# Kernel tuning notes

Measured on AMD Instinct MI355X. Metric: run time of the kernel, lower is better.

Reference implementation:

```python
import jax, jax.numpy as jnp
import numpy as np

H, F = 4, 32          # num_of_heads, num_out_features
HF = H * F            # 128
F_IN = 128
EDGE_DIM = 64
HIDDEN = 256
B = 64
MLE = 1500
N = B * MLE           # 96000
E = 600000
LN_EPS = 1e-5


def setup_inputs() -> dict:
    key = jax.random.key(0)
    ks = jax.random.split(key, 20)

    def glorot(k, shape):
        fan_in, fan_out = shape[-2], shape[-1]
        lim = np.sqrt(6.0 / (fan_in + fan_out))
        return jax.random.uniform(k, shape, jnp.float32, -lim, lim)

    inp = {
        "in_nodes_features": jax.random.normal(ks[0], (N, F_IN), jnp.float32),
        "edge_index": jax.random.randint(ks[1], (2, E), 0, N),
        "edges": jax.random.normal(ks[2], (E, EDGE_DIM), jnp.float32),
        "instructions": jax.random.normal(ks[3], (B, HIDDEN), jnp.float32),
        "batch_ids": jax.random.randint(ks[4], (E,), 0, B),
        "max_local_entity": MLE,
        # parameters (stored as [in, out]; torch Linear is x @ W.T)
        "W_proj": glorot(ks[5], (F_IN, HF)),
        "W_edge": glorot(ks[6], (EDGE_DIM, HF)),
        "W_src_ins": glorot(ks[7], (HIDDEN, HF)),
        "b_src_ins": jnp.zeros((HF,), jnp.float32),
        "W_trg_ins": glorot(ks[8], (HIDDEN, HF)),
        "b_trg_ins": jnp.zeros((HF,), jnp.float32),
        "W_edge_ins": glorot(ks[9], (HIDDEN, HF)),
        "b_edge_ins": jnp.zeros((HF,), jnp.float32),
        "a_src": glorot(ks[10], (1, H, F)),
        "a_trg": glorot(ks[11], (1, H, F)),
        "a_edge": glorot(ks[12], (1, H, F)),
        "bias": jnp.zeros((HF,), jnp.float32),
        "W_skip": glorot(ks[13], (F_IN, HF)),
        "ln_gamma": jnp.ones((2 * HF,), jnp.float32),
        "ln_beta": jnp.zeros((2 * HF,), jnp.float32),
    }
    return inp


def _segment_softmax(scores, seg_idx, num_nodes):
    # scores: [E, H]; softmax over edges sharing the same seg_idx node
    s = scores - jax.lax.stop_gradient(scores.max())  # global-max shift, as in original
    e = jnp.exp(s)
    denom = jax.ops.segment_sum(e, seg_idx, num_segments=num_nodes)  # [N, H]
    return (e / (denom[seg_idx] + 1e-16))[..., None]  # [E, H, 1]


def _branch(proj, lift_idx, agg_idx, scores_per_edge, x, W_skip, bias, num_nodes):
    att = _segment_softmax(scores_per_edge, agg_idx, num_nodes)          # [E,H,1]
    weighted = proj[lift_idx] * att                                      # [E,H,F]
    out = jax.ops.segment_sum(weighted, agg_idx, num_segments=num_nodes) # [N,H,F]
    out = out + (x @ W_skip).reshape(num_nodes, H, F)                    # skip (F != F_in path)
    out = out.reshape(num_nodes, HF) + bias                              # concat heads + bias
    return out


def reference(in_nodes_features, edge_index, edges, instructions, batch_ids,
              max_local_entity, W_proj, W_edge, W_src_ins, b_src_ins,
              W_trg_ins, b_trg_ins, W_edge_ins, b_edge_ins,
              a_src, a_trg, a_edge, bias, W_skip, ln_gamma, ln_beta):
    x = in_nodes_features                      # dropout disabled (eval / p=0)
    num_nodes = x.shape[0]
    b = instructions.shape[0]
    src_idx, trg_idx = edge_index[0], edge_index[1]

    proj = (x @ W_proj).reshape(num_nodes, H, F)           # [N,H,F]
    eproj = (edges @ W_edge).reshape(-1, H, F)             # [E,H,F]

    def bridge(Wi, bi):  # instruction -> per-node [N,H,F]
        br = instructions @ Wi + bi                        # [B,HF]
        br = jnp.broadcast_to(br[:, None, :], (b, max_local_entity, HF))
        return br.reshape(num_nodes, H, F)

    src_br = bridge(W_src_ins, b_src_ins)
    trg_br = bridge(W_trg_ins, b_trg_ins)
    edge_br = (instructions @ W_edge_ins + b_edge_ins)[batch_ids].reshape(-1, H, F)

    scores_source = (proj * a_src * src_br).sum(-1)        # [N,H]
    scores_target = (proj * a_trg * trg_br).sum(-1)        # [N,H]
    scores_edge = (eproj * a_edge * edge_br).sum(-1)       # [E,H]

    scores_per_edge = jax.nn.leaky_relu(
        scores_source[src_idx] + scores_target[trg_idx] + scores_edge,
        negative_slope=0.2)                                # [E,H]

    # direction == 'all': aggregate src->trg and trg->src
    trg_feats = _branch(proj, src_idx, trg_idx, scores_per_edge, x, W_skip, bias, num_nodes)
    src_feats = _branch(proj, trg_idx, src_idx, scores_per_edge, x, W_skip, bias, num_nodes)

    out = jnp.concatenate([src_feats, trg_feats], axis=1)  # [N, 2*HF]
    mu = out.mean(-1, keepdims=True)
    var = ((out - mu) ** 2).mean(-1, keepdims=True)
    return (out - mu) * jax.lax.rsqrt(var + LN_EPS) * ln_gamma + ln_beta
```

## Files before the change

### kernel.cpp

```cpp
#include <hip/hip_runtime.h>
#include <stdint.h>

typedef unsigned short ushortT;
typedef __attribute__((ext_vector_type(8))) short short8;
typedef __attribute__((ext_vector_type(4))) float float4_;

#define HH 4
#define FF 32
#define HFD 128
#define F_IN 128
#define EDGE_DIM 64
#define HIDDEN 256
#define BB 64
#define MLE 1500
#define NN 96000
#define EEc 600000
#define CAP 32

__device__ __forceinline__ float bf_lo(uint32_t u){ return __uint_as_float(u << 16); }
__device__ __forceinline__ float bf_hi(uint32_t u){ return __uint_as_float(u & 0xffff0000u); }
__device__ __forceinline__ uint32_t f2bf(float f){
    uint32_t u = __float_as_uint(f);
    return (u + 0x7fffu + ((u >> 16) & 1u)) >> 16;
}
__device__ __forceinline__ short8 cvt8(const float* p){
    float4_ x0 = *(const float4_*)p;
    float4_ x1 = *(const float4_*)(p + 4);
    short8 r;
    r[0]=(short)f2bf(x0[0]); r[1]=(short)f2bf(x0[1]); r[2]=(short)f2bf(x0[2]); r[3]=(short)f2bf(x0[3]);
    r[4]=(short)f2bf(x1[0]); r[5]=(short)f2bf(x1[1]); r[6]=(short)f2bf(x1[2]); r[7]=(short)f2bf(x1[3]);
    return r;
}

__global__ void k_bridge(const float* ins, const float* Wsrc, const float* bsrc,
                         const float* Wtrg, const float* btrg,
                         const float* Wedg, const float* bedg,
                         const float* a_src, const float* a_trg, const float* a_edge,
                         const float* W_edge,
                         float* csrc, float* ctrg, float* Mout)
{
    __shared__ float ins_s[HIDDEN];
    __shared__ float ce_s[HFD];
    int b = blockIdx.x, t = threadIdx.x;
    const float* ip = ins + b * HIDDEN;
    ins_s[t]       = ip[t];
    ins_s[t + 128] = ip[t + 128];
    __syncthreads();
    float as = 0.f, at = 0.f, ae = 0.f;
    for (int k = 0; k < HIDDEN; k++){
        float iv = ins_s[k];
        as += iv * Wsrc[k*HFD + t];
        at += iv * Wtrg[k*HFD + t];
        ae += iv * Wedg[k*HFD + t];
    }
    csrc[b*HFD + t] = (as + bsrc[t]) * a_src[t];
    ctrg[b*HFD + t] = (at + btrg[t]) * a_trg[t];
    ce_s[t] = (ae + bedg[t]) * a_edge[t];
    __syncthreads();
    #pragma unroll
    for (int rep = 0; rep < 2; rep++){
        int idx = t + rep * 128;
        int d = idx >> 2, h = idx & 3;
        float acc = 0.f;
        #pragma unroll
        for (int f = 0; f < FF; f++)
            acc += W_edge[d*HFD + h*FF + f] * ce_s[h*FF + f];
        Mout[b*256 + h*64 + d] = acc;
    }
}

__global__ void k_transpose(const float* Wp, const float* Wsk, ushortT* WcatT)
{
    int idx = blockIdx.x * 256 + threadIdx.x;
    int c = idx >> 7;
    int d = idx & 127;
    float v = (c < 128) ? Wp[d*128 + c] : Wsk[d*128 + (c - 128)];
    WcatT[c*128 + d] = (ushortT)f2bf(v);
}

__global__ __launch_bounds__(256) void k_gemm(const float* x, const ushortT* WcatT,
                                              const float* csrc, const float* ctrg,
                                              ushortT* proj, ushortT* skip,
                                              float* s_src, float* s_trg)
{
    int t = threadIdx.x;
    int w = t >> 6, lane = t & 63;
    int q = lane >> 4, n16 = lane & 15;
    size_t node = (size_t)blockIdx.x * 64 + w * 16 + n16;

    float4_ acc[16];
    #pragma unroll
    for (int j = 0; j < 16; j++) acc[j] = (float4_){0.f, 0.f, 0.f, 0.f};

    #pragma unroll
    for (int kk = 0; kk < 4; kk++){
        short8 bfrag = cvt8(x + node * 128 + kk*32 + q*8);
        #pragma unroll
        for (int j = 0; j < 16; j++){
            short8 afrag = *(const short8*)(WcatT + (size_t)(j*16 + n16) * 128 + kk*32 + q*8);
            acc[j] = __builtin_amdgcn_mfma_f32_16x16x32_bf16(afrag, bfrag, acc[j], 0, 0, 0);
        }
    }

    #pragma unroll
    for (int j = 0; j < 16; j++){
        uint32_t p0 = f2bf(acc[j][0]) | (f2bf(acc[j][1]) << 16);
        uint32_t p1 = f2bf(acc[j][2]) | (f2bf(acc[j][3]) << 16);
        ushortT* base = (j < 8) ? (proj + node*128 + j*16 + q*4)
                                : (skip + node*128 + (j-8)*16 + q*4);
        uint2 pv; pv.x = p0; pv.y = p1;
        *(uint2*)base = pv;
    }

    int b = (int)(node / MLE);
    const float* cs = csrc + b * HFD;
    const float* ct = ctrg + b * HFD;
    float ps[4] = {0,0,0,0}, pt[4] = {0,0,0,0};
    #pragma unroll
    for (int j = 0; j < 8; j++){
        int h = j >> 1;
        #pragma unroll
        for (int r = 0; r < 4; r++){
            int c = j*16 + q*4 + r;
            ps[h] += acc[j][r] * cs[c];
            pt[h] += acc[j][r] * ct[c];
        }
    }
    #pragma unroll
    for (int m = 16; m < 64; m <<= 1){
        #pragma unroll
        for (int hh = 0; hh < 4; hh++){
            ps[hh] += __shfl_xor(ps[hh], m, 64);
            pt[hh] += __shfl_xor(pt[hh], m, 64);
        }
    }
    float vs = (q == 0) ? ps[0] : (q == 1) ? ps[1] : (q == 2) ? ps[2] : ps[3];
    float vt = (q == 0) ? pt[0] : (q == 1) ? pt[1] : (q == 2) ? pt[2] : pt[3];
    s_src[node*4 + q] = vs;
    s_trg[node*4 + q] = vt;
}

__global__ __launch_bounds__(256) void k_edges(const int* eidx, const int* bids,
    const float* edges, const float* M, const float* s_src, const float* s_trg,
    float* ex, int* cnt_src, int* cnt_trg, uint32_t* adj_src, uint32_t* adj_trg)
{
    int t = threadIdx.x;
    int wave = t >> 6, l = t & 63;
    int g = l >> 4, s = l & 15;
    int eb = (blockIdx.x * 4 + wave) * 16;

    float4_ ev[4];
    int bidv[4];
    #pragma unroll
    for (int i = 0; i < 4; i++){
        int r = i*4 + g;
        ev[i]   = *(const float4_*)(edges + (size_t)(eb + r) * 64 + s*4);
        bidv[i] = bids[eb + r];
    }

    float p00=0.f,p01=0.f,p02=0.f,p03=0.f;
    float p10=0.f,p11=0.f,p12=0.f,p13=0.f;
    float p20=0.f,p21=0.f,p22=0.f,p23=0.f;
    float p30=0.f,p31=0.f,p32=0.f,p33=0.f;
    #pragma unroll
    for (int i = 0; i < 4; i++){
        const float* Mb = M + (size_t)bidv[i] * 256;
        float4_ m0 = *(const float4_*)(Mb +   0 + s*4);
        float4_ m1 = *(const float4_*)(Mb +  64 + s*4);
        float4_ m2 = *(const float4_*)(Mb + 128 + s*4);
        float4_ m3 = *(const float4_*)(Mb + 192 + s*4);
        float4_ e4 = ev[i];
        float d0 = e4[0]*m0[0] + e4[1]*m0[1] + e4[2]*m0[2] + e4[3]*m0[3];
        float d1 = e4[0]*m1[0] + e4[1]*m1[1] + e4[2]*m1[2] + e4[3]*m1[3];
        float d2 = e4[0]*m2[0] + e4[1]*m2[1] + e4[2]*m2[2] + e4[3]*m2[3];
        float d3 = e4[0]*m3[0] + e4[1]*m3[1] + e4[2]*m3[2] + e4[3]*m3[3];
        if (i == 0){ p00=d0; p01=d1; p02=d2; p03=d3; }
        if (i == 1){ p10=d0; p11=d1; p12=d2; p13=d3; }
        if (i == 2){ p20=d0; p21=d1; p22=d2; p23=d3; }
        if (i == 3){ p30=d0; p31=d1; p32=d2; p33=d3; }
    }

    #pragma unroll
    for (int mm = 1; mm < 16; mm <<= 1){
        p00 += __shfl_xor(p00, mm, 64); p01 += __shfl_xor(p01, mm, 64);
        p02 += __shfl_xor(p02, mm, 64); p03 += __shfl_xor(p03, mm, 64);
        p10 += __shfl_xor(p10, mm, 64); p11 += __shfl_xor(p11, mm, 64);
        p12 += __shfl_xor(p12, mm, 64); p13 += __shfl_xor(p13, mm, 64);
        p20 += __shfl_xor(p20, mm, 64); p21 += __shfl_xor(p21, mm, 64);
        p22 += __shfl_xor(p22, mm, 64); p23 += __shfl_xor(p23, mm, 64);
        p30 += __shfl_xor(p30, mm, 64); p31 += __shfl_xor(p31, mm, 64);
        p32 += __shfl_xor(p32, mm, 64); p33 += __shfl_xor(p33, mm, 64);
    }

    int i_sel = s >> 2;
    int h_sel = s & 3;
    float q0 = h_sel==0 ? p00 : h_sel==1 ? p01 : h_sel==2 ? p02 : p03;
    float q1 = h_sel==0 ? p10 : h_sel==1 ? p11 : h_sel==2 ? p12 : p13;
    float q2 = h_sel==0 ? p20 : h_sel==1 ? p21 : h_sel==2 ? p22 : p23;
    float q3 = h_sel==0 ? p30 : h_sel==1 ? p31 : h_sel==2 ? p32 : p33;
    float se = i_sel==0 ? q0 : i_sel==1 ? q1 : i_sel==2 ? q2 : q3;

    int e   = eb + i_sel*4 + g;
    int src = eidx[e];
    int trg = eidx[EEc + e];
    float sc = s_src[(size_t)src*4 + h_sel] + s_trg[(size_t)trg*4 + h_sel] + se;
    sc = sc > 0.f ? sc : 0.2f * sc;
    ex[(size_t)e*4 + h_sel] = __expf(sc);

    if (h_sel == 0){
        int sl = atomicAdd(&cnt_src[src], 1);
        if (sl < CAP) adj_src[(size_t)src*CAP + sl] = (uint32_t)e;
        int sl2 = atomicAdd(&cnt_trg[trg], 1);
        if (sl2 < CAP) adj_trg[(size_t)trg*CAP + sl2] = (uint32_t)e;
    }
}

__global__ __launch_bounds__(256) void k_agg(const ushortT* proj, const ushortT* skip,
    const float* bias, const float* ex, const int* eidx,
    const int* cnt_src, const int* cnt_trg,
    const uint32_t* adj_src, const uint32_t* adj_trg,
    const float* gamma, const float* beta, float* out)
{
    __shared__ int   sh_nbr[2][4][CAP];
    __shared__ float sh_ev [2][4][CAP*4];

    int wave = threadIdx.x >> 6, lane = threadIdx.x & 63;
    int n = blockIdx.x * 4 + wave;
    int h = lane >> 4;

    int cnt0 = cnt_src[n]; if (cnt0 > CAP) cnt0 = CAP;
    int cnt1 = cnt_trg[n]; if (cnt1 > CAP) cnt1 = CAP;

    if (lane < cnt0){
        int e = (int)adj_src[(size_t)n * CAP + lane];
        sh_nbr[0][wave][lane] = eidx[EEc + e];
        *(float4_*)&sh_ev[0][wave][lane*4] = *(const float4_*)(ex + (size_t)e*4);
    }
    if (lane < cnt1){
        int e = (int)adj_trg[(size_t)n * CAP + lane];
        sh_nbr[1][wave][lane] = eidx[e];
        *(float4_*)&sh_ev[1][wave][lane*4] = *(const float4_*)(ex + (size_t)e*4);
    }

    uint32_t sv = ((const uint32_t*)(skip + (size_t)n * 128))[lane];
    float b0 = bias[2*lane], b1 = bias[2*lane + 1];

    __syncthreads();

    float sk0 = bf_lo(sv) + b0;
    float sk1 = bf_hi(sv) + b1;

    float a0 = 0.f, a1 = 0.f, ad = 0.f;
    #pragma unroll 4
    for (int i = 0; i < cnt0; i++){
        int nbr  = sh_nbr[0][wave][i];
        float ev = sh_ev[0][wave][i*4 + h];
        uint32_t pv = ((const uint32_t*)(proj + (size_t)nbr * 128))[lane];
        a0 += ev * bf_lo(pv);
        a1 += ev * bf_hi(pv);
        ad += ev;
    }
    float inv = 1.f / (ad + 1e-16f);
    float f0 = a0 * inv + sk0;
    float f1 = a1 * inv + sk1;

    a0 = 0.f; a1 = 0.f; ad = 0.f;
    #pragma unroll 4
    for (int i = 0; i < cnt1; i++){
        int nbr  = sh_nbr[1][wave][i];
        float ev = sh_ev[1][wave][i*4 + h];
        uint32_t pv = ((const uint32_t*)(proj + (size_t)nbr * 128))[lane];
        a0 += ev * bf_lo(pv);
        a1 += ev * bf_hi(pv);
        ad += ev;
    }
    inv = 1.f / (ad + 1e-16f);
    float f2 = a0 * inv + sk0;
    float f3 = a1 * inv + sk1;

    float sum  = f0 + f1 + f2 + f3;
    float sq = f0*f0 + f1*f1 + f2*f2 + f3*f3;
    #pragma unroll
    for (int m = 1; m < 64; m <<= 1){
        sum += __shfl_xor(sum, m, 64);
        sq  += __shfl_xor(sq,  m, 64);
    }
    float mu  = sum * (1.f/256.f);
    float var = sq * (1.f/256.f) - mu*mu;
    var = var < 0.f ? 0.f : var;
    float rr = rsqrtf(var + 1e-5f);

    float o0 = (f0 - mu) * rr * gamma[2*lane]           + beta[2*lane];
    float o1 = (f1 - mu) * rr * gamma[2*lane + 1]       + beta[2*lane + 1];
    float o2 = (f2 - mu) * rr * gamma[128 + 2*lane]     + beta[128 + 2*lane];
    float o3 = (f3 - mu) * rr * gamma[128 + 2*lane + 1] + beta[128 + 2*lane + 1];

    float* orow = out + (size_t)n * 256;
    *(float2*)(orow + 2*lane)       = make_float2(o0, o1);
    *(float2*)(orow + 128 + 2*lane) = make_float2(o2, o3);
}

extern "C" void kernel_launch(void* const* d_in, const int* in_sizes, int n_in,
                              void* d_out, int out_size, void* d_ws, size_t ws_size,
                              hipStream_t stream)
{
    const float* x      = (const float*)d_in[0];
    const int*   eidx   = (const int*)d_in[1];
    const float* edges  = (const float*)d_in[2];
    const float* ins    = (const float*)d_in[3];
    const int*   bids   = (const int*)d_in[4];
    const float* Wproj  = (const float*)d_in[6];
    const float* Wedge  = (const float*)d_in[7];
    const float* Wsrc   = (const float*)d_in[8];
    const float* bsrc   = (const float*)d_in[9];
    const float* Wtrg   = (const float*)d_in[10];
    const float* btrg   = (const float*)d_in[11];
    const float* Wedgi  = (const float*)d_in[12];
    const float* bedgi  = (const float*)d_in[13];
    const float* a_src  = (const float*)d_in[14];
    const float* a_trg  = (const float*)d_in[15];
    const float* a_edge = (const float*)d_in[16];
    const float* bias   = (const float*)d_in[17];
    const float* Wskip  = (const float*)d_in[18];
    const float* gamma  = (const float*)d_in[19];
    const float* beta   = (const float*)d_in[20];

    char* ws = (char*)d_ws;
    size_t off = 0;
    ushortT* proj  = (ushortT*)(ws + off); off += (size_t)NN * 128 * 2;
    ushortT* skip  = (ushortT*)(ws + off); off += (size_t)NN * 128 * 2;
    ushortT* WcatT = (ushortT*)(ws + off); off += 256 * 128 * 2;
    float*   csrc  = (float*)(ws + off);   off += BB * HFD * 4;
    float*   ctrg  = (float*)(ws + off);   off += BB * HFD * 4;
    float*   M     = (float*)(ws + off);   off += BB * 256 * 4;
    float*   s_src = (float*)(ws + off);   off += (size_t)NN * 4 * 4;
    float*   s_trg = (float*)(ws + off);   off += (size_t)NN * 4 * 4;
    float*   ex    = (float*)(ws + off);   off += (size_t)EEc * 4 * 4;
    int*     cnt_src = (int*)(ws + off);   off += (size_t)NN * 4;
    int*     cnt_trg = (int*)(ws + off);   off += (size_t)NN * 4;
    uint32_t* adj_src = (uint32_t*)(ws + off); off += (size_t)NN * CAP * 4;
    uint32_t* adj_trg = (uint32_t*)(ws + off); off += (size_t)NN * CAP * 4;

    hipMemsetAsync(cnt_src, 0, (size_t)NN * 4 * 2, stream);

    k_bridge<<<dim3(BB), dim3(128), 0, stream>>>(ins, Wsrc, bsrc, Wtrg, btrg, Wedgi, bedgi,
                                                 a_src, a_trg, a_edge, Wedge, csrc, ctrg, M);
    k_transpose<<<dim3(128), dim3(256), 0, stream>>>(Wproj, Wskip, WcatT);
    k_gemm<<<dim3(NN/64), dim3(256), 0, stream>>>(x, WcatT, csrc, ctrg, proj, skip, s_src, s_trg);
    k_edges<<<dim3(EEc/64), dim3(256), 0, stream>>>(eidx, bids, edges, M, s_src, s_trg,
                                                    ex, cnt_src, cnt_trg, adj_src, adj_trg);
    k_agg<<<dim3(NN/4), dim3(256), 0, stream>>>(proj, skip, bias, ex, eidx, cnt_src, cnt_trg,
                                                adj_src, adj_trg, gamma, beta, (float*)d_out);
}
```

Measured before the change: 556.7 us.

## Pack neighbor id and bf16 edge weights into adjacency entries; interleave both aggregation loops

After: 564.8 us. Within noise of the previous version (+1.5%).

```diff
diff --git a/kernel.cpp b/kernel.cpp
--- a/kernel.cpp
+++ b/kernel.cpp
@@ -142,7 +142,7 @@
 
 __global__ __launch_bounds__(256) void k_edges(const int* eidx, const int* bids,
     const float* edges, const float* M, const float* s_src, const float* s_trg,
-    float* ex, int* cnt_src, int* cnt_trg, uint32_t* adj_src, uint32_t* adj_trg)
+    int* cnt_src, int* cnt_trg, uint4* adj_src, uint4* adj_trg)
 {
     int t = threadIdx.x;
     int wave = t >> 6, l = t & 63;
@@ -205,20 +205,32 @@
     int trg = eidx[EEc + e];
     float sc = s_src[(size_t)src*4 + h_sel] + s_trg[(size_t)trg*4 + h_sel] + se;
     sc = sc > 0.f ? sc : 0.2f * sc;
-    ex[(size_t)e*4 + h_sel] = __expf(sc);
+    float exv = __expf(sc);
+
+    uint32_t my   = f2bf(exv) << ((h_sel & 1) * 16);
+    uint32_t pair = my | __shfl_xor(my, 1, 64);
+    uint32_t both = __shfl_xor(pair, 2, 64);
 
     if (h_sel == 0){
+        uint4 ent;
+        ent.y = pair; ent.z = both; ent.w = 0u;
         int sl = atomicAdd(&cnt_src[src], 1);
-        if (sl < CAP) adj_src[(size_t)src*CAP + sl] = (uint32_t)e;
+        if (sl < CAP){
+            ent.x = (uint32_t)trg;
+            adj_src[(size_t)src*CAP + sl] = ent;
+        }
         int sl2 = atomicAdd(&cnt_trg[trg], 1);
-        if (sl2 < CAP) adj_trg[(size_t)trg*CAP + sl2] = (uint32_t)e;
+        if (sl2 < CAP){
+            ent.x = (uint32_t)src;
+            adj_trg[(size_t)trg*CAP + sl2] = ent;
+        }
     }
 }
 
 __global__ __launch_bounds__(256) void k_agg(const ushortT* proj, const ushortT* skip,
-    const float* bias, const float* ex, const int* eidx,
+    const float* bias,
     const int* cnt_src, const int* cnt_trg,
-    const uint32_t* adj_src, const uint32_t* adj_trg,
+    const uint4* adj_src, const uint4* adj_trg,
     const float* gamma, const float* beta, float* out)
 {
     __shared__ int   sh_nbr[2][4][CAP];
@@ -232,14 +244,16 @@
     int cnt1 = cnt_trg[n]; if (cnt1 > CAP) cnt1 = CAP;
 
     if (lane < cnt0){
-        int e = (int)adj_src[(size_t)n * CAP + lane];
-        sh_nbr[0][wave][lane] = eidx[EEc + e];
-        *(float4_*)&sh_ev[0][wave][lane*4] = *(const float4_*)(ex + (size_t)e*4);
+        uint4 ent = adj_src[(size_t)n * CAP + lane];
+        sh_nbr[0][wave][lane] = (int)ent.x;
+        float4_ evv = { bf_lo(ent.y), bf_hi(ent.y), bf_lo(ent.z), bf_hi(ent.z) };
+        *(float4_*)&sh_ev[0][wave][lane*4] = evv;
     }
     if (lane < cnt1){
-        int e = (int)adj_trg[(size_t)n * CAP + lane];
-        sh_nbr[1][wave][lane] = eidx[e];
-        *(float4_*)&sh_ev[1][wave][lane*4] = *(const float4_*)(ex + (size_t)e*4);
+        uint4 ent = adj_trg[(size_t)n * CAP + lane];
+        sh_nbr[1][wave][lane] = (int)ent.x;
+        float4_ evv = { bf_lo(ent.y), bf_hi(ent.y), bf_lo(ent.z), bf_hi(ent.z) };
+        *(float4_*)&sh_ev[1][wave][lane*4] = evv;
     }
 
     uint32_t sv = ((const uint32_t*)(skip + (size_t)n * 128))[lane];
@@ -251,35 +265,36 @@
     float sk1 = bf_hi(sv) + b1;
 
     float a0 = 0.f, a1 = 0.f, ad = 0.f;
-    #pragma unroll 4
-    for (int i = 0; i < cnt0; i++){
-        int nbr  = sh_nbr[0][wave][i];
-        float ev = sh_ev[0][wave][i*4 + h];
-        uint32_t pv = ((const uint32_t*)(proj + (size_t)nbr * 128))[lane];
-        a0 += ev * bf_lo(pv);
-        a1 += ev * bf_hi(pv);
-        ad += ev;
+    float c0 = 0.f, c1 = 0.f, cd = 0.f;
+    int cmax = cnt0 > cnt1 ? cnt0 : cnt1;
+    #pragma unroll 2
+    for (int i = 0; i < cmax; i++){
+        if (i < cnt0){
+            int nbr  = sh_nbr[0][wave][i];
+            float evw = sh_ev[0][wave][i*4 + h];
+            uint32_t pv = ((const uint32_t*)(proj + (size_t)nbr * 128))[lane];
+            a0 += evw * bf_lo(pv);
+            a1 += evw * bf_hi(pv);
+            ad += evw;
+        }
+        if (i < cnt1){
+            int nbr  = sh_nbr[1][wave][i];
+            float evw = sh_ev[1][wave][i*4 + h];
+            uint32_t pv = ((const uint32_t*)(proj + (size_t)nbr * 128))[lane];
+            c0 += evw * bf_lo(pv);
+            c1 += evw * bf_hi(pv);
+            cd += evw;
+        }
     }
     float inv = 1.f / (ad + 1e-16f);
     float f0 = a0 * inv + sk0;
     float f1 = a1 * inv + sk1;
-
-    a0 = 0.f; a1 = 0.f; ad = 0.f;
-    #pragma unroll 4
-    for (int i = 0; i < cnt1; i++){
-        int nbr  = sh_nbr[1][wave][i];
-        float ev = sh_ev[1][wave][i*4 + h];
-        uint32_t pv = ((const uint32_t*)(proj + (size_t)nbr * 128))[lane];
-        a0 += ev * bf_lo(pv);
-        a1 += ev * bf_hi(pv);
-        ad += ev;
-    }
-    inv = 1.f / (ad + 1e-16f);
-    float f2 = a0 * inv + sk0;
-    float f3 = a1 * inv + sk1;
-
-    float sum  = f0 + f1 + f2 + f3;
-    float sq = f0*f0 + f1*f1 + f2*f2 + f3*f3;
+    inv = 1.f / (cd + 1e-16f);
+    float f2 = c0 * inv + sk0;
+    float f3 = c1 * inv + sk1;
+
+    float sum = f0 + f1 + f2 + f3;
+    float sq  = f0*f0 + f1*f1 + f2*f2 + f3*f3;
     #pragma unroll
     for (int m = 1; m < 64; m <<= 1){
         sum += __shfl_xor(sum, m, 64);
@@ -335,11 +350,10 @@
     float*   M     = (float*)(ws + off);   off += BB * 256 * 4;
     float*   s_src = (float*)(ws + off);   off += (size_t)NN * 4 * 4;
     float*   s_trg = (float*)(ws + off);   off += (size_t)NN * 4 * 4;
-    float*   ex    = (float*)(ws + off);   off += (size_t)EEc * 4 * 4;
     int*     cnt_src = (int*)(ws + off);   off += (size_t)NN * 4;
     int*     cnt_trg = (int*)(ws + off);   off += (size_t)NN * 4;
-    uint32_t* adj_src = (uint32_t*)(ws + off); off += (size_t)NN * CAP * 4;
-    uint32_t* adj_trg = (uint32_t*)(ws + off); off += (size_t)NN * CAP * 4;
+    uint4*   adj_src = (uint4*)(ws + off); off += (size_t)NN * CAP * 16;
+    uint4*   adj_trg = (uint4*)(ws + off); off += (size_t)NN * CAP * 16;
 
     hipMemsetAsync(cnt_src, 0, (size_t)NN * 4 * 2, stream);
 
@@ -348,7 +362,7 @@
     k_transpose<<<dim3(128), dim3(256), 0, stream>>>(Wproj, Wskip, WcatT);
     k_gemm<<<dim3(NN/64), dim3(256), 0, stream>>>(x, WcatT, csrc, ctrg, proj, skip, s_src, s_trg);
     k_edges<<<dim3(EEc/64), dim3(256), 0, stream>>>(eidx, bids, edges, M, s_src, s_trg,
-                                                    ex, cnt_src, cnt_trg, adj_src, adj_trg);
-    k_agg<<<dim3(NN/4), dim3(256), 0, stream>>>(proj, skip, bias, ex, eidx, cnt_src, cnt_trg,
+                                                    cnt_src, cnt_trg, adj_src, adj_trg);
+    k_agg<<<dim3(NN/4), dim3(256), 0, stream>>>(proj, skip, bias, cnt_src, cnt_trg,
                                                 adj_src, adj_trg, gamma, beta, (float*)d_out);
 }
```
